# Performance work log

Hardware: AMD Instinct MI355X
Metric: run time of the kernel (lower is better)

## Reference

```python
import jax, jax.numpy as jnp
import numpy as np

CHAN = 256
KEY_DIM = 64
VALUE_DIM = 64
HEADS = 8


def _conv1x1(x, W, b):
    # x: [b,c,h,w], W: [out,c], b: [out]  (1x1 conv == channel matmul)
    return jnp.einsum('bchw,oc->bohw', x, W) + b[None, :, None, None]


def setup_inputs() -> dict:
    key = jax.random.key(0)
    ks = jax.random.split(key, 9)
    qk_out = KEY_DIM * HEADS
    v_out = VALUE_DIM * HEADS
    s_in = 1.0 / np.sqrt(CHAN)
    s_out = 1.0 / np.sqrt(v_out)
    return {
        'x': jax.random.normal(ks[0], (16, CHAN, 64, 64), dtype=jnp.float32),
        'Wq': jax.random.uniform(ks[1], (qk_out, CHAN), jnp.float32, -s_in, s_in),
        'bq': jax.random.uniform(ks[2], (qk_out,), jnp.float32, -s_in, s_in),
        'Wk': jax.random.uniform(ks[3], (qk_out, CHAN), jnp.float32, -s_in, s_in),
        'bk': jax.random.uniform(ks[4], (qk_out,), jnp.float32, -s_in, s_in),
        'Wv': jax.random.uniform(ks[5], (v_out, CHAN), jnp.float32, -s_in, s_in),
        'bv': jax.random.uniform(ks[6], (v_out,), jnp.float32, -s_in, s_in),
        'Wo': jax.random.uniform(ks[7], (CHAN, v_out), jnp.float32, -s_out, s_out),
        'bo': jax.random.uniform(ks[8], (CHAN,), jnp.float32, -s_out, s_out),
    }


def reference(x, Wq, bq, Wk, bk, Wv, bv, Wo, bo):
    b, c, h, w = x.shape
    n = h * w
    scale = KEY_DIM ** (-0.25)
    q = _conv1x1(x, Wq, bq).reshape(b, HEADS, KEY_DIM, n) * scale
    k = _conv1x1(x, Wk, bk).reshape(b, HEADS, KEY_DIM, n) * scale
    v = _conv1x1(x, Wv, bv).reshape(b, HEADS, VALUE_DIM, n)
    k = jax.nn.softmax(k, axis=-1)       # over positions n
    q = jax.nn.softmax(q, axis=-2)       # over key_dim d (norm_queries=True)
    ctx = jnp.einsum('bhdn,bhen->bhde', k, v)   # [b,h,d,e] small context
    out = jnp.einsum('bhdn,bhde->bhen', q, ctx) # [b,h,e,n]
    out = out.reshape(b, HEADS * VALUE_DIM, h, w)
    return _conv1x1(out, Wo, bo)
```

## Files before the change

### kernel.cpp

```cpp
#include <hip/hip_runtime.h>
#include <hip/hip_bf16.h>

typedef unsigned short u16;
typedef unsigned int u32;
typedef __attribute__((ext_vector_type(8))) short bf16x8;
typedef __attribute__((ext_vector_type(4))) float f32x4;

#define NB 16
#define NHEADS 8
#define NPOS 4096
#define QK_SCALE 0.35355339059327373f

__device__ __forceinline__ float bf2f(u32 u) {
  union { u32 i; float f; } x; x.i = u << 16; return x.f;
}
__device__ __forceinline__ u16 f2bf(float f) {
  union { float f; u32 i; } x; x.f = f;
  u32 r = x.i + 0x7fffu + ((x.i >> 16) & 1u);
  return (u16)(r >> 16);
}
__device__ __forceinline__ void unpack8(uint4 r, float* v) {
  v[0] = bf2f(r.x & 0xffffu); v[1] = bf2f(r.x >> 16);
  v[2] = bf2f(r.y & 0xffffu); v[3] = bf2f(r.y >> 16);
  v[4] = bf2f(r.z & 0xffffu); v[5] = bf2f(r.z >> 16);
  v[6] = bf2f(r.w & 0xffffu); v[7] = bf2f(r.w >> 16);
}

__device__ __forceinline__ void async16(u16* ldst, const u16* gsrc) {
  __builtin_amdgcn_global_load_lds(
      (const __attribute__((address_space(1))) unsigned int*)gsrc,
      (__attribute__((address_space(3))) unsigned int*)ldst, 16, 0, 0);
}

__global__ __launch_bounds__(256) void transpose_x(const float* __restrict__ x,
                                                   u16* __restrict__ xT) {
  int b = blockIdx.z;
  int c0 = blockIdx.y * 64;
  int n0 = blockIdx.x * 64;
  const float* xp = x + ((long)b * 256 + c0) * 4096 + n0;
  u16* op = xT + ((long)b * 4096 + n0) * 256 + c0;
  __shared__ float T[64][65];
  int t = threadIdx.x;
  {
    int cl = t >> 2, nc = (t & 3) * 16;
    #pragma unroll
    for (int u = 0; u < 4; ++u) {
      float4 v = *(const float4*)&xp[(long)cl * 4096 + nc + u * 4];
      T[nc + u*4 + 0][cl] = v.x; T[nc + u*4 + 1][cl] = v.y;
      T[nc + u*4 + 2][cl] = v.z; T[nc + u*4 + 3][cl] = v.w;
    }
  }
  __syncthreads();
  {
    int nl = t >> 2, cc = (t & 3) * 16;
    u32 wv[8];
    #pragma unroll
    for (int j = 0; j < 8; ++j)
      wv[j] = (u32)f2bf(T[nl][cc + 2*j]) | ((u32)f2bf(T[nl][cc + 2*j + 1]) << 16);
    *(uint4*)&op[(long)nl * 256 + cc]     = make_uint4(wv[0], wv[1], wv[2], wv[3]);
    *(uint4*)&op[(long)nl * 256 + cc + 8] = make_uint4(wv[4], wv[5], wv[6], wv[7]);
  }
}

__global__ __launch_bounds__(256) void convert_w(
    const float* __restrict__ w0, const float* __restrict__ w1, const float* __restrict__ w2,
    u16* __restrict__ o0, u16* __restrict__ o1, u16* __restrict__ o2) {
  int gid = blockIdx.x * 256 + threadIdx.x;
  int which = gid >> 13;
  int off = (gid & 8191) * 16;
  const float* src = (which == 0) ? w0 : (which == 1) ? w1 : w2;
  u16* dst = (which == 0) ? o0 : (which == 1) ? o1 : o2;
  u32 wv[8];
  #pragma unroll
  for (int u = 0; u < 2; ++u) {
    float4 a = *(const float4*)&src[off + u*8];
    float4 b = *(const float4*)&src[off + u*8 + 4];
    wv[u*4+0] = (u32)f2bf(a.x) | ((u32)f2bf(a.y) << 16);
    wv[u*4+1] = (u32)f2bf(a.z) | ((u32)f2bf(a.w) << 16);
    wv[u*4+2] = (u32)f2bf(b.x) | ((u32)f2bf(b.y) << 16);
    wv[u*4+3] = (u32)f2bf(b.z) | ((u32)f2bf(b.w) << 16);
  }
  *(uint4*)&dst[off]     = make_uint4(wv[0], wv[1], wv[2], wv[3]);
  *(uint4*)&dst[off + 8] = make_uint4(wv[4], wv[5], wv[6], wv[7]);
}

template<int OUT_MODE>
__global__ __launch_bounds__(256) void mfma_gemm(
    const u16* __restrict__ A, long aBatch,
    const u16* __restrict__ B, long bBatch,
    const float* __restrict__ bias,
    void* __restrict__ Cv, long cBatch,
    int K, float scale)
{
  int b = blockIdx.z;
  A += (long)b * aBatch;
  B += (long)b * bBatch;
  int m0 = blockIdx.y * 128, n0 = blockIdx.x * 128;

  __shared__ u16 sm[16384];
  int t = threadIdx.x, w = t >> 6, l = t & 63;
  int lr = l & 15, lk = l >> 4;
  int wr = w >> 1, wcq = w & 1;

  f32x4 acc[4][4];
  #pragma unroll
  for (int i = 0; i < 4; ++i)
    #pragma unroll
    for (int j = 0; j < 4; ++j)
      acc[i][j] = (f32x4){0.f, 0.f, 0.f, 0.f};

  int srow8 = l >> 3;
  int ksl = ((l & 7) ^ (l >> 3)) * 8;

  int nkt = K >> 6;
  for (int kt = 0; kt < nkt; ++kt) {
    int k0 = kt << 6;
    __syncthreads();
    #pragma unroll
    for (int i = 0; i < 4; ++i) {
      int seg = w * 4 + i;
      int row = seg * 8 + srow8;
      async16(&sm[seg * 512], A + (long)(m0 + row) * K + k0 + ksl);
    }
    #pragma unroll
    for (int i = 0; i < 4; ++i) {
      int seg = w * 4 + i;
      int row = seg * 8 + srow8;
      async16(&sm[8192 + seg * 512], B + (long)(n0 + row) * K + k0 + ksl);
    }
    __syncthreads();
    #pragma unroll
    for (int s = 0; s < 2; ++s) {
      bf16x8 af[4], bf[4];
      #pragma unroll
      for (int mi = 0; mi < 4; ++mi) {
        int row = wr * 64 + mi * 16 + lr;
        int slot = (s * 4 + lk) ^ (row & 7);
        af[mi] = *(const bf16x8*)&sm[row * 64 + slot * 8];
      }
      #pragma unroll
      for (int ni = 0; ni < 4; ++ni) {
        int row = wcq * 64 + ni * 16 + lr;
        int slot = (s * 4 + lk) ^ (row & 7);
        bf[ni] = *(const bf16x8*)&sm[8192 + row * 64 + slot * 8];
      }
      #pragma unroll
      for (int mi = 0; mi < 4; ++mi)
        #pragma unroll
        for (int ni = 0; ni < 4; ++ni)
          acc[mi][ni] = __builtin_amdgcn_mfma_f32_16x16x32_bf16(af[mi], bf[ni], acc[mi][ni], 0, 0, 0);
    }
  }

  if (OUT_MODE == 1) {
    u16* Cq = (u16*)Cv + (long)b * cBatch;
    #pragma unroll
    for (int mi = 0; mi < 4; ++mi) {
      int mb = m0 + wr * 64 + mi * 16 + lk * 4;
      float b0 = bias[mb], b1 = bias[mb+1], b2 = bias[mb+2], b3 = bias[mb+3];
      #pragma unroll
      for (int ni = 0; ni < 4; ++ni) {
        int n = n0 + wcq * 64 + ni * 16 + lr;
        f32x4 v = acc[mi][ni];
        ushort4 o;
        o.x = f2bf((v[0] + b0) * scale); o.y = f2bf((v[1] + b1) * scale);
        o.z = f2bf((v[2] + b2) * scale); o.w = f2bf((v[3] + b3) * scale);
        *(ushort4*)&Cq[(long)n * 512 + mb] = o;
      }
    }
  } else if (OUT_MODE == 0) {
    u16* Cb = (u16*)Cv + (long)b * cBatch;
    #pragma unroll
    for (int mi = 0; mi < 4; ++mi)
      #pragma unroll
      for (int r = 0; r < 4; ++r) {
        int m = m0 + wr * 64 + mi * 16 + lk * 4 + r;
        float bi = bias[m];
        #pragma unroll
        for (int ni = 0; ni < 4; ++ni) {
          int n = n0 + wcq * 64 + ni * 16 + lr;
          Cb[(long)m * NPOS + n] = f2bf((acc[mi][ni][r] + bi) * scale);
        }
      }
  } else {
    float* Cf = (float*)Cv + (long)b * cBatch;
    #pragma unroll
    for (int mi = 0; mi < 4; ++mi)
      #pragma unroll
      for (int r = 0; r < 4; ++r) {
        int m = m0 + wr * 64 + mi * 16 + lk * 4 + r;
        float bi = bias[m];
        #pragma unroll
        for (int ni = 0; ni < 4; ++ni) {
          int n = n0 + wcq * 64 + ni * 16 + lr;
          Cf[(long)m * NPOS + n] = acc[mi][ni][r] + bi;
        }
      }
  }
}

__global__ __launch_bounds__(256) void softmax_n(u16* __restrict__ kd) {
  long row = blockIdx.x;
  u16* p = kd + row * NPOS;
  int tid = threadIdx.x;
  int lane = tid & 63, wid = tid >> 6;

  float v[16];
  uint4 r0 = *(const uint4*)(p + tid * 16);
  uint4 r1 = *(const uint4*)(p + tid * 16 + 8);
  unpack8(r0, v); unpack8(r1, v + 8);

  float mx = -1e30f;
  #pragma unroll
  for (int u = 0; u < 16; ++u) mx = fmaxf(mx, v[u]);
  #pragma unroll
  for (int off = 32; off > 0; off >>= 1) mx = fmaxf(mx, __shfl_xor(mx, off));
  __shared__ float smx[4], ssum[4];
  if (lane == 0) smx[wid] = mx;
  __syncthreads();
  mx = fmaxf(fmaxf(smx[0], smx[1]), fmaxf(smx[2], smx[3]));

  float s = 0.f;
  #pragma unroll
  for (int u = 0; u < 16; ++u) { v[u] = __expf(v[u] - mx); s += v[u]; }
  #pragma unroll
  for (int off = 32; off > 0; off >>= 1) s += __shfl_xor(s, off);
  if (lane == 0) ssum[wid] = s;
  __syncthreads();
  s = ssum[0] + ssum[1] + ssum[2] + ssum[3];
  float inv = 1.f / s;

  uint4 o0, o1;
  o0.x = (u32)f2bf(v[0]*inv)  | ((u32)f2bf(v[1]*inv)  << 16);
  o0.y = (u32)f2bf(v[2]*inv)  | ((u32)f2bf(v[3]*inv)  << 16);
  o0.z = (u32)f2bf(v[4]*inv)  | ((u32)f2bf(v[5]*inv)  << 16);
  o0.w = (u32)f2bf(v[6]*inv)  | ((u32)f2bf(v[7]*inv)  << 16);
  o1.x = (u32)f2bf(v[8]*inv)  | ((u32)f2bf(v[9]*inv)  << 16);
  o1.y = (u32)f2bf(v[10]*inv) | ((u32)f2bf(v[11]*inv) << 16);
  o1.z = (u32)f2bf(v[12]*inv) | ((u32)f2bf(v[13]*inv) << 16);
  o1.w = (u32)f2bf(v[14]*inv) | ((u32)f2bf(v[15]*inv) << 16);
  *(uint4*)(p + tid * 16) = o0;
  *(uint4*)(p + tid * 16 + 8) = o1;
}

__global__ __launch_bounds__(64) void ctx_mfma(
    const u16* __restrict__ ksm, const u16* __restrict__ vv, float* __restrict__ ctxp) {
  int ns = blockIdx.x;
  int bh = blockIdx.y;
  const u16* kp = ksm + (long)bh * 64 * NPOS + ns * 256;
  const u16* vp = vv  + (long)bh * 64 * NPOS + ns * 256;
  int l = threadIdx.x;
  int lr = l & 15, lk = l >> 4;
  f32x4 acc[4][4];
  #pragma unroll
  for (int i = 0; i < 4; ++i)
    #pragma unroll
    for (int j = 0; j < 4; ++j)
      acc[i][j] = (f32x4){0.f, 0.f, 0.f, 0.f};

  #pragma unroll 2
  for (int s = 0; s < 8; ++s) {
    int nn = s * 32 + lk * 8;
    bf16x8 a[4], bb[4];
    #pragma unroll
    for (int mi = 0; mi < 4; ++mi)
      a[mi] = *(const bf16x8*)(kp + (long)(mi * 16 + lr) * NPOS + nn);
    #pragma unroll
    for (int ni = 0; ni < 4; ++ni)
      bb[ni] = *(const bf16x8*)(vp + (long)(ni * 16 + lr) * NPOS + nn);
    #pragma unroll
    for (int mi = 0; mi < 4; ++mi)
      #pragma unroll
      for (int ni = 0; ni < 4; ++ni)
        acc[mi][ni] = __builtin_amdgcn_mfma_f32_16x16x32_bf16(a[mi], bb[ni], acc[mi][ni], 0, 0, 0);
  }
  float* cp = ctxp + ((long)ns * 128 + bh) * 4096;
  #pragma unroll
  for (int mi = 0; mi < 4; ++mi)
    #pragma unroll
    for (int ni = 0; ni < 4; ++ni)
      #pragma unroll
      for (int r = 0; r < 4; ++r)
        cp[(mi * 16 + lk * 4 + r) * 64 + ni * 16 + lr] = acc[mi][ni][r];
}

__global__ __launch_bounds__(256) void wc_kernel(
    const float* __restrict__ ctxp, const float* __restrict__ Wo, u16* __restrict__ Wc)
{
  int bh = blockIdx.x;
  int bb = bh >> 3, h = bh & 7;
  __shared__ float Cs[64][65];
  __shared__ float Ws[64][65];
  int tid = threadIdx.x, tx = tid & 15, ty = tid >> 4;

  {
    int row = tid >> 2;
    int ec  = (tid & 3) << 4;
    #pragma unroll
    for (int u = 0; u < 4; ++u) {
      float4 s = make_float4(0, 0, 0, 0);
      #pragma unroll
      for (int si = 0; si < 16; ++si) {
        float4 tv = *(const float4*)&ctxp[(((long)si * 128 + bh) * 64 + row) * 64 + ec + u * 4];
        s.x += tv.x; s.y += tv.y; s.z += tv.z; s.w += tv.w;
      }
      Cs[row][ec + u*4 + 0] = s.x; Cs[row][ec + u*4 + 1] = s.y;
      Cs[row][ec + u*4 + 2] = s.z; Cs[row][ec + u*4 + 3] = s.w;
    }
  }
  for (int cc = 0; cc < 4; ++cc) {
    __syncthreads();
    {
      int row = tid >> 2;
      int ec  = (tid & 3) << 4;
      #pragma unroll
      for (int u = 0; u < 4; ++u) {
        float4 wv = *(const float4*)&Wo[(long)(cc * 64 + row) * 512 + h * 64 + ec + u * 4];
        Ws[row][ec + u*4 + 0] = wv.x; Ws[row][ec + u*4 + 1] = wv.y;
        Ws[row][ec + u*4 + 2] = wv.z; Ws[row][ec + u*4 + 3] = wv.w;
      }
    }
    __syncthreads();
    float acc[4][4] = {};
    #pragma unroll 8
    for (int e = 0; e < 64; ++e) {
      float a[4], b[4];
      #pragma unroll
      for (int i = 0; i < 4; ++i) a[i] = Ws[(ty << 2) + i][e];
      #pragma unroll
      for (int j = 0; j < 4; ++j) b[j] = Cs[(tx << 2) + j][e];
      #pragma unroll
      for (int i = 0; i < 4; ++i)
        #pragma unroll
        for (int j = 0; j < 4; ++j)
          acc[i][j] += a[i] * b[j];
    }
    #pragma unroll
    for (int i = 0; i < 4; ++i) {
      int co = cc * 64 + (ty << 2) + i;
      ushort4 o;
      o.x = f2bf(acc[i][0]); o.y = f2bf(acc[i][1]);
      o.z = f2bf(acc[i][2]); o.w = f2bf(acc[i][3]);
      *(ushort4*)&Wc[((long)bb * 256 + co) * 512 + h * 64 + (tx << 2)] = o;
    }
  }
}

__global__ __launch_bounds__(256) void softmax_d_t(u16* __restrict__ qT) {
  long gid = (long)blockIdx.x * 256 + threadIdx.x;
  u16* p = qT + gid * 64;
  float v[64];
  #pragma unroll
  for (int u = 0; u < 8; ++u) {
    uint4 r = *(const uint4*)(p + u * 8);
    unpack8(r, v + u * 8);
  }
  float mx = -1e30f;
  #pragma unroll
  for (int d = 0; d < 64; ++d) mx = fmaxf(mx, v[d]);
  float s = 0.f;
  #pragma unroll
  for (int d = 0; d < 64; ++d) { v[d] = __expf(v[d] - mx); s += v[d]; }
  float inv = 1.f / s;
  #pragma unroll
  for (int u = 0; u < 8; ++u) {
    uint4 o;
    o.x = (u32)f2bf(v[u*8+0]*inv) | ((u32)f2bf(v[u*8+1]*inv) << 16);
    o.y = (u32)f2bf(v[u*8+2]*inv) | ((u32)f2bf(v[u*8+3]*inv) << 16);
    o.z = (u32)f2bf(v[u*8+4]*inv) | ((u32)f2bf(v[u*8+5]*inv) << 16);
    o.w = (u32)f2bf(v[u*8+6]*inv) | ((u32)f2bf(v[u*8+7]*inv) << 16);
    *(uint4*)(p + u * 8) = o;
  }
}

extern "C" void kernel_launch(void* const* d_in, const int* in_sizes, int n_in,
                              void* d_out, int out_size, void* d_ws, size_t ws_size,
                              hipStream_t stream) {
  (void)in_sizes; (void)n_in; (void)out_size; (void)ws_size;
  const float* x  = (const float*)d_in[0];
  const float* Wq = (const float*)d_in[1];
  const float* bq = (const float*)d_in[2];
  const float* Wk = (const float*)d_in[3];
  const float* bk = (const float*)d_in[4];
  const float* Wv = (const float*)d_in[5];
  const float* bv = (const float*)d_in[6];
  const float* Wo = (const float*)d_in[7];
  const float* bo = (const float*)d_in[8];
  float* out = (float*)d_out;

  char* ws = (char*)d_ws;
  u16*   xT   = (u16*)(ws);
  float* ctxp = (float*)(ws);
  u16*   qT   = (u16*)(ws + 33554432L);
  u16*   kb   = (u16*)(ws + 100663296L);
  u16*   Wcb  = (u16*)(ws + 167772160L);
  u16*   Wqb  = (u16*)(ws + 171966464L);
  u16*   Wkb  = (u16*)(ws + 172228608L);
  u16*   Wvb  = (u16*)(ws + 172490752L);
  u16*   vb   = (u16*)d_out;

  dim3 blk(256);
  long bBx = (long)NPOS * 256;
  long cBqkv = (long)512 * NPOS;
  long cBqT = (long)NPOS * 512;

  hipLaunchKernelGGL(transpose_x, dim3(64, 4, NB), blk, 0, stream, x, xT);
  hipLaunchKernelGGL(convert_w, dim3(96), blk, 0, stream, Wq, Wk, Wv, Wqb, Wkb, Wvb);

  hipLaunchKernelGGL(HIP_KERNEL_NAME(mfma_gemm<1>), dim3(32, 4, NB), blk, 0, stream,
                     Wqb, 0L, xT, bBx, bq, (void*)qT, cBqT, 256, QK_SCALE);
  hipLaunchKernelGGL(HIP_KERNEL_NAME(mfma_gemm<0>), dim3(32, 4, NB), blk, 0, stream,
                     Wkb, 0L, xT, bBx, bk, (void*)kb, cBqkv, 256, QK_SCALE);
  hipLaunchKernelGGL(HIP_KERNEL_NAME(mfma_gemm<0>), dim3(32, 4, NB), blk, 0, stream,
                     Wvb, 0L, xT, bBx, bv, (void*)vb, cBqkv, 256, 1.0f);

  hipLaunchKernelGGL(softmax_n, dim3(NB * 512), blk, 0, stream, kb);
  hipLaunchKernelGGL(ctx_mfma, dim3(16, NB * NHEADS), dim3(64), 0, stream, kb, vb, ctxp);
  hipLaunchKernelGGL(wc_kernel, dim3(NB * NHEADS), blk, 0, stream, ctxp, Wo, Wcb);
  hipLaunchKernelGGL(softmax_d_t, dim3(NB * NPOS * NHEADS / 256), blk, 0, stream, qT);

  hipLaunchKernelGGL(HIP_KERNEL_NAME(mfma_gemm<2>), dim3(32, 2, NB), blk, 0, stream,
                     Wcb, (long)256 * 512, qT, cBqT, bo, (void*)out, (long)256 * NPOS,
                     512, 1.0f);
}
```

Before: 359.4 us.

## Fuse QKV projections with softmaxes and defer key normalization into context

Merges the three QKV projection GEMMs into one launch with a concatenated weight matrix that has the scale folded in. The query softmax over key_dim is computed in the GEMM epilogue via cross-lane shuffles, and the key softmax's exponent is applied there too. The key normalizer is accumulated with an MFMA against a ones vector in the context kernel and divided out in wc_kernel. This removes the separate softmax passes and their round trips through memory. Both GEMMs also gain double-buffered LDS staging. Skipping the max subtraction risks exp overflow for large keys, and bf16 storage of unnormalized exponentials loses some precision.

```diff
diff --git a/kernel.cpp b/kernel.cpp
--- a/kernel.cpp
+++ b/kernel.cpp
@@ -7,7 +7,6 @@
 typedef __attribute__((ext_vector_type(4))) float f32x4;
 
 #define NB 16
-#define NHEADS 8
 #define NPOS 4096
 #define QK_SCALE 0.35355339059327373f
 
@@ -18,12 +17,6 @@
   union { float f; u32 i; } x; x.f = f;
   u32 r = x.i + 0x7fffu + ((x.i >> 16) & 1u);
   return (u16)(r >> 16);
-}
-__device__ __forceinline__ void unpack8(uint4 r, float* v) {
-  v[0] = bf2f(r.x & 0xffffu); v[1] = bf2f(r.x >> 16);
-  v[2] = bf2f(r.y & 0xffffu); v[3] = bf2f(r.y >> 16);
-  v[4] = bf2f(r.z & 0xffffu); v[5] = bf2f(r.z >> 16);
-  v[6] = bf2f(r.w & 0xffffu); v[7] = bf2f(r.w >> 16);
 }
 
 __device__ __forceinline__ void async16(u16* ldst, const u16* gsrc) {
@@ -62,201 +55,198 @@
   }
 }
 
-__global__ __launch_bounds__(256) void convert_w(
-    const float* __restrict__ w0, const float* __restrict__ w1, const float* __restrict__ w2,
-    u16* __restrict__ o0, u16* __restrict__ o1, u16* __restrict__ o2) {
-  int gid = blockIdx.x * 256 + threadIdx.x;
-  int which = gid >> 13;
-  int off = (gid & 8191) * 16;
-  const float* src = (which == 0) ? w0 : (which == 1) ? w1 : w2;
-  u16* dst = (which == 0) ? o0 : (which == 1) ? o1 : o2;
-  u32 wv[8];
-  #pragma unroll
-  for (int u = 0; u < 2; ++u) {
-    float4 a = *(const float4*)&src[off + u*8];
-    float4 b = *(const float4*)&src[off + u*8 + 4];
-    wv[u*4+0] = (u32)f2bf(a.x) | ((u32)f2bf(a.y) << 16);
-    wv[u*4+1] = (u32)f2bf(a.z) | ((u32)f2bf(a.w) << 16);
-    wv[u*4+2] = (u32)f2bf(b.x) | ((u32)f2bf(b.y) << 16);
-    wv[u*4+3] = (u32)f2bf(b.z) | ((u32)f2bf(b.w) << 16);
-  }
-  *(uint4*)&dst[off]     = make_uint4(wv[0], wv[1], wv[2], wv[3]);
-  *(uint4*)&dst[off + 8] = make_uint4(wv[4], wv[5], wv[6], wv[7]);
-}
-
-template<int OUT_MODE>
-__global__ __launch_bounds__(256) void mfma_gemm(
-    const u16* __restrict__ A, long aBatch,
-    const u16* __restrict__ B, long bBatch,
-    const float* __restrict__ bias,
-    void* __restrict__ Cv, long cBatch,
-    int K, float scale)
+__global__ __launch_bounds__(256) void convert_wqkv(
+    const float* __restrict__ Wq, const float* __restrict__ Wk, const float* __restrict__ Wv,
+    const float* __restrict__ bq, const float* __restrict__ bk, const float* __restrict__ bv,
+    u16* __restrict__ W, float* __restrict__ bias)
+{
+  if (blockIdx.x < 96) {
+    int gid = blockIdx.x * 256 + threadIdx.x;
+    int which = gid >> 13;
+    int off = (gid & 8191) * 16;
+    const float* src = which == 0 ? Wq : which == 1 ? Wk : Wv;
+    float scl = which == 2 ? 1.0f : QK_SCALE;
+    u16* dst = W + which * 131072;
+    u32 wv_[8];
+    #pragma unroll
+    for (int u = 0; u < 4; ++u) {
+      float4 a = *(const float4*)&src[off + u * 4];
+      wv_[u*2+0] = (u32)f2bf(a.x*scl) | ((u32)f2bf(a.y*scl) << 16);
+      wv_[u*2+1] = (u32)f2bf(a.z*scl) | ((u32)f2bf(a.w*scl) << 16);
+    }
+    *(uint4*)&dst[off]     = make_uint4(wv_[0], wv_[1], wv_[2], wv_[3]);
+    *(uint4*)&dst[off + 8] = make_uint4(wv_[4], wv_[5], wv_[6], wv_[7]);
+  } else {
+    int t = threadIdx.x;
+    #pragma unroll
+    for (int u = 0; u < 6; ++u) {
+      int i = t * 6 + u;
+      if (i < 1536) {
+        int which = i >> 9, r = i & 511;
+        float v = which == 0 ? bq[r] : which == 1 ? bk[r] : bv[r];
+        bias[i] = which == 2 ? v : v * QK_SCALE;
+      }
+    }
+  }
+}
+
+__global__ __launch_bounds__(256) void proj_qkv(
+    const u16* __restrict__ W, const float* __restrict__ bias,
+    const u16* __restrict__ xT, u16* __restrict__ qT,
+    u16* __restrict__ kx, u16* __restrict__ vb)
 {
   int b = blockIdx.z;
-  A += (long)b * aBatch;
-  B += (long)b * bBatch;
-  int m0 = blockIdx.y * 128, n0 = blockIdx.x * 128;
-
-  __shared__ u16 sm[16384];
+  const u16* Bm = xT + (long)b * (4096L * 256);
+  int mb = blockIdx.y;
+  int m0 = mb * 128, n0 = blockIdx.x * 128;
+
+  __shared__ u16 sm[32768];
   int t = threadIdx.x, w = t >> 6, l = t & 63;
   int lr = l & 15, lk = l >> 4;
   int wr = w >> 1, wcq = w & 1;
+  int srow8 = l >> 3;
+  int ksl = ((l & 7) ^ srow8) * 8;
 
   f32x4 acc[4][4];
   #pragma unroll
   for (int i = 0; i < 4; ++i)
     #pragma unroll
-    for (int j = 0; j < 4; ++j)
-      acc[i][j] = (f32x4){0.f, 0.f, 0.f, 0.f};
-
-  int srow8 = l >> 3;
-  int ksl = ((l & 7) ^ (l >> 3)) * 8;
-
-  int nkt = K >> 6;
-  for (int kt = 0; kt < nkt; ++kt) {
-    int k0 = kt << 6;
-    __syncthreads();
-    #pragma unroll
-    for (int i = 0; i < 4; ++i) {
-      int seg = w * 4 + i;
-      int row = seg * 8 + srow8;
-      async16(&sm[seg * 512], A + (long)(m0 + row) * K + k0 + ksl);
-    }
-    #pragma unroll
-    for (int i = 0; i < 4; ++i) {
-      int seg = w * 4 + i;
-      int row = seg * 8 + srow8;
-      async16(&sm[8192 + seg * 512], B + (long)(n0 + row) * K + k0 + ksl);
-    }
-    __syncthreads();
-    #pragma unroll
-    for (int s = 0; s < 2; ++s) {
-      bf16x8 af[4], bf[4];
-      #pragma unroll
-      for (int mi = 0; mi < 4; ++mi) {
-        int row = wr * 64 + mi * 16 + lr;
-        int slot = (s * 4 + lk) ^ (row & 7);
-        af[mi] = *(const bf16x8*)&sm[row * 64 + slot * 8];
-      }
-      #pragma unroll
-      for (int ni = 0; ni < 4; ++ni) {
-        int row = wcq * 64 + ni * 16 + lr;
-        int slot = (s * 4 + lk) ^ (row & 7);
-        bf[ni] = *(const bf16x8*)&sm[8192 + row * 64 + slot * 8];
-      }
+    for (int j = 0; j < 4; ++j) acc[i][j] = (f32x4){0.f, 0.f, 0.f, 0.f};
+
+#define STAGE_P(buf, kt) { \
+    u16* base_ = sm + (buf) * 16384; \
+    int k0_ = (kt) * 64; \
+    _Pragma("unroll") \
+    for (int i_ = 0; i_ < 4; ++i_) { \
+      int seg_ = w * 4 + i_; \
+      int row_ = seg_ * 8 + srow8; \
+      async16(base_ + seg_ * 512, W + (long)(m0 + row_) * 256 + k0_ + ksl); \
+      async16(base_ + 8192 + seg_ * 512, Bm + (long)(n0 + row_) * 256 + k0_ + ksl); \
+    } }
+
+#define COMPUTE_P(buf) { \
+    const u16* base_ = sm + (buf) * 16384; \
+    _Pragma("unroll") \
+    for (int s_ = 0; s_ < 2; ++s_) { \
+      bf16x8 af_[4], bf_[4]; \
+      _Pragma("unroll") \
+      for (int mi_ = 0; mi_ < 4; ++mi_) { \
+        int row_ = wr * 64 + mi_ * 16 + lr; \
+        int slot_ = (s_ * 4 + lk) ^ (row_ & 7); \
+        af_[mi_] = *(const bf16x8*)&base_[row_ * 64 + slot_ * 8]; \
+      } \
+      _Pragma("unroll") \
+      for (int ni_ = 0; ni_ < 4; ++ni_) { \
+        int row_ = wcq * 64 + ni_ * 16 + lr; \
+        int slot_ = (s_ * 4 + lk) ^ (row_ & 7); \
+        bf_[ni_] = *(const bf16x8*)&base_[8192 + row_ * 64 + slot_ * 8]; \
+      } \
+      _Pragma("unroll") \
+      for (int mi_ = 0; mi_ < 4; ++mi_) \
+        _Pragma("unroll") \
+        for (int ni_ = 0; ni_ < 4; ++ni_) \
+          acc[mi_][ni_] = __builtin_amdgcn_mfma_f32_16x16x32_bf16(af_[mi_], bf_[ni_], acc[mi_][ni_], 0, 0, 0); \
+    } }
+
+#define WAITBAR asm volatile("s_waitcnt vmcnt(0)" ::: "memory"); __builtin_amdgcn_s_barrier();
+
+  STAGE_P(0, 0)
+  WAITBAR
+  STAGE_P(1, 1)
+  COMPUTE_P(0)
+  WAITBAR
+  STAGE_P(0, 2)
+  COMPUTE_P(1)
+  WAITBAR
+  STAGE_P(1, 3)
+  COMPUTE_P(0)
+  WAITBAR
+  COMPUTE_P(1)
+
+  int mbase = m0 + wr * 64;
+  int nbase = n0 + wcq * 64;
+
+  if (mb < 4) {
+    float bv_[4][4];
+    #pragma unroll
+    for (int mi = 0; mi < 4; ++mi)
+      #pragma unroll
+      for (int r = 0; r < 4; ++r) bv_[mi][r] = bias[mbase + mi * 16 + lk * 4 + r];
+    u16* qp = qT + (long)b * (4096L * 512);
+    #pragma unroll
+    for (int ni = 0; ni < 4; ++ni) {
+      float ssum = 0.f;
       #pragma unroll
       for (int mi = 0; mi < 4; ++mi)
         #pragma unroll
-        for (int ni = 0; ni < 4; ++ni)
-          acc[mi][ni] = __builtin_amdgcn_mfma_f32_16x16x32_bf16(af[mi], bf[ni], acc[mi][ni], 0, 0, 0);
-    }
-  }
-
-  if (OUT_MODE == 1) {
-    u16* Cq = (u16*)Cv + (long)b * cBatch;
-    #pragma unroll
-    for (int mi = 0; mi < 4; ++mi) {
-      int mb = m0 + wr * 64 + mi * 16 + lk * 4;
-      float b0 = bias[mb], b1 = bias[mb+1], b2 = bias[mb+2], b3 = bias[mb+3];
-      #pragma unroll
-      for (int ni = 0; ni < 4; ++ni) {
-        int n = n0 + wcq * 64 + ni * 16 + lr;
-        f32x4 v = acc[mi][ni];
+        for (int r = 0; r < 4; ++r) {
+          float e = __expf(acc[mi][ni][r] + bv_[mi][r]);
+          acc[mi][ni][r] = e; ssum += e;
+        }
+      ssum += __shfl_xor(ssum, 16);
+      ssum += __shfl_xor(ssum, 32);
+      float inv = 1.f / ssum;
+      int n = nbase + ni * 16 + lr;
+      #pragma unroll
+      for (int mi = 0; mi < 4; ++mi) {
         ushort4 o;
-        o.x = f2bf((v[0] + b0) * scale); o.y = f2bf((v[1] + b1) * scale);
-        o.z = f2bf((v[2] + b2) * scale); o.w = f2bf((v[3] + b3) * scale);
-        *(ushort4*)&Cq[(long)n * 512 + mb] = o;
-      }
-    }
-  } else if (OUT_MODE == 0) {
-    u16* Cb = (u16*)Cv + (long)b * cBatch;
+        o.x = f2bf(acc[mi][ni][0] * inv); o.y = f2bf(acc[mi][ni][1] * inv);
+        o.z = f2bf(acc[mi][ni][2] * inv); o.w = f2bf(acc[mi][ni][3] * inv);
+        *(ushort4*)&qp[(long)n * 512 + mbase + mi * 16 + lk * 4] = o;
+      }
+    }
+  } else if (mb < 8) {
+    u16* kp = kx + (long)b * (512L * 4096) + (long)(mbase - 512) * 4096;
     #pragma unroll
     for (int mi = 0; mi < 4; ++mi)
       #pragma unroll
       for (int r = 0; r < 4; ++r) {
-        int m = m0 + wr * 64 + mi * 16 + lk * 4 + r;
-        float bi = bias[m];
+        int mr = mi * 16 + lk * 4 + r;
+        float bi = bias[mbase + mr];
         #pragma unroll
         for (int ni = 0; ni < 4; ++ni) {
-          int n = n0 + wcq * 64 + ni * 16 + lr;
-          Cb[(long)m * NPOS + n] = f2bf((acc[mi][ni][r] + bi) * scale);
+          int n = nbase + ni * 16 + lr;
+          kp[(long)mr * 4096 + n] = f2bf(__expf(acc[mi][ni][r] + bi));
         }
       }
   } else {
-    float* Cf = (float*)Cv + (long)b * cBatch;
+    u16* vp = vb + (long)b * (512L * 4096) + (long)(mbase - 1024) * 4096;
     #pragma unroll
     for (int mi = 0; mi < 4; ++mi)
       #pragma unroll
       for (int r = 0; r < 4; ++r) {
-        int m = m0 + wr * 64 + mi * 16 + lk * 4 + r;
-        float bi = bias[m];
+        int mr = mi * 16 + lk * 4 + r;
+        float bi = bias[mbase + mr];
         #pragma unroll
         for (int ni = 0; ni < 4; ++ni) {
-          int n = n0 + wcq * 64 + ni * 16 + lr;
-          Cf[(long)m * NPOS + n] = acc[mi][ni][r] + bi;
+          int n = nbase + ni * 16 + lr;
+          vp[(long)mr * 4096 + n] = f2bf(acc[mi][ni][r] + bi);
         }
       }
   }
-}
-
-__global__ __launch_bounds__(256) void softmax_n(u16* __restrict__ kd) {
-  long row = blockIdx.x;
-  u16* p = kd + row * NPOS;
-  int tid = threadIdx.x;
-  int lane = tid & 63, wid = tid >> 6;
-
-  float v[16];
-  uint4 r0 = *(const uint4*)(p + tid * 16);
-  uint4 r1 = *(const uint4*)(p + tid * 16 + 8);
-  unpack8(r0, v); unpack8(r1, v + 8);
-
-  float mx = -1e30f;
-  #pragma unroll
-  for (int u = 0; u < 16; ++u) mx = fmaxf(mx, v[u]);
-  #pragma unroll
-  for (int off = 32; off > 0; off >>= 1) mx = fmaxf(mx, __shfl_xor(mx, off));
-  __shared__ float smx[4], ssum[4];
-  if (lane == 0) smx[wid] = mx;
-  __syncthreads();
-  mx = fmaxf(fmaxf(smx[0], smx[1]), fmaxf(smx[2], smx[3]));
-
-  float s = 0.f;
-  #pragma unroll
-  for (int u = 0; u < 16; ++u) { v[u] = __expf(v[u] - mx); s += v[u]; }
-  #pragma unroll
-  for (int off = 32; off > 0; off >>= 1) s += __shfl_xor(s, off);
-  if (lane == 0) ssum[wid] = s;
-  __syncthreads();
-  s = ssum[0] + ssum[1] + ssum[2] + ssum[3];
-  float inv = 1.f / s;
-
-  uint4 o0, o1;
-  o0.x = (u32)f2bf(v[0]*inv)  | ((u32)f2bf(v[1]*inv)  << 16);
-  o0.y = (u32)f2bf(v[2]*inv)  | ((u32)f2bf(v[3]*inv)  << 16);
-  o0.z = (u32)f2bf(v[4]*inv)  | ((u32)f2bf(v[5]*inv)  << 16);
-  o0.w = (u32)f2bf(v[6]*inv)  | ((u32)f2bf(v[7]*inv)  << 16);
-  o1.x = (u32)f2bf(v[8]*inv)  | ((u32)f2bf(v[9]*inv)  << 16);
-  o1.y = (u32)f2bf(v[10]*inv) | ((u32)f2bf(v[11]*inv) << 16);
-  o1.z = (u32)f2bf(v[12]*inv) | ((u32)f2bf(v[13]*inv) << 16);
-  o1.w = (u32)f2bf(v[14]*inv) | ((u32)f2bf(v[15]*inv) << 16);
-  *(uint4*)(p + tid * 16) = o0;
-  *(uint4*)(p + tid * 16 + 8) = o1;
+#undef STAGE_P
+#undef COMPUTE_P
 }
 
 __global__ __launch_bounds__(64) void ctx_mfma(
-    const u16* __restrict__ ksm, const u16* __restrict__ vv, float* __restrict__ ctxp) {
+    const u16* __restrict__ kx, const u16* __restrict__ vv,
+    float* __restrict__ Sp, float* __restrict__ Zp)
+{
   int ns = blockIdx.x;
   int bh = blockIdx.y;
-  const u16* kp = ksm + (long)bh * 64 * NPOS + ns * 256;
-  const u16* vp = vv  + (long)bh * 64 * NPOS + ns * 256;
-  int l = threadIdx.x;
-  int lr = l & 15, lk = l >> 4;
-  f32x4 acc[4][4];
-  #pragma unroll
-  for (int i = 0; i < 4; ++i)
-    #pragma unroll
-    for (int j = 0; j < 4; ++j)
-      acc[i][j] = (f32x4){0.f, 0.f, 0.f, 0.f};
+  const u16* kp = kx + (long)bh * 64 * NPOS + ns * 256;
+  const u16* vp = vv + (long)bh * 64 * NPOS + ns * 256;
+  int l = threadIdx.x, lr = l & 15, lk = l >> 4;
+  f32x4 acc[4][4]; f32x4 az[4];
+  #pragma unroll
+  for (int i = 0; i < 4; ++i) {
+    az[i] = (f32x4){0.f, 0.f, 0.f, 0.f};
+    #pragma unroll
+    for (int j = 0; j < 4; ++j) acc[i][j] = (f32x4){0.f, 0.f, 0.f, 0.f};
+  }
+  bf16x8 ones;
+  #pragma unroll
+  for (int j = 0; j < 8; ++j) ones[j] = (short)0x3F80;
 
   #pragma unroll 2
   for (int s = 0; s < 8; ++s) {
@@ -270,22 +260,34 @@
       bb[ni] = *(const bf16x8*)(vp + (long)(ni * 16 + lr) * NPOS + nn);
     #pragma unroll
     for (int mi = 0; mi < 4; ++mi)
+      az[mi] = __builtin_amdgcn_mfma_f32_16x16x32_bf16(a[mi], ones, az[mi], 0, 0, 0);
+    #pragma unroll
+    for (int mi = 0; mi < 4; ++mi)
       #pragma unroll
       for (int ni = 0; ni < 4; ++ni)
         acc[mi][ni] = __builtin_amdgcn_mfma_f32_16x16x32_bf16(a[mi], bb[ni], acc[mi][ni], 0, 0, 0);
   }
-  float* cp = ctxp + ((long)ns * 128 + bh) * 4096;
+  float* sp = Sp + ((long)ns * 128 + bh) * 4096;
   #pragma unroll
   for (int mi = 0; mi < 4; ++mi)
     #pragma unroll
     for (int ni = 0; ni < 4; ++ni)
       #pragma unroll
       for (int r = 0; r < 4; ++r)
-        cp[(mi * 16 + lk * 4 + r) * 64 + ni * 16 + lr] = acc[mi][ni][r];
+        sp[(mi * 16 + lk * 4 + r) * 64 + ni * 16 + lr] = acc[mi][ni][r];
+  if (lr == 0) {
+    float* zp = Zp + ((long)ns * 128 + bh) * 64;
+    #pragma unroll
+    for (int mi = 0; mi < 4; ++mi)
+      #pragma unroll
+      for (int r = 0; r < 4; ++r)
+        zp[mi * 16 + lk * 4 + r] = az[mi][r];
+  }
 }
 
 __global__ __launch_bounds__(256) void wc_kernel(
-    const float* __restrict__ ctxp, const float* __restrict__ Wo, u16* __restrict__ Wc)
+    const float* __restrict__ Sp, const float* __restrict__ Zp,
+    const float* __restrict__ Wo, u16* __restrict__ Wc)
 {
   int bh = blockIdx.x;
   int bb = bh >> 3, h = bh & 7;
@@ -296,16 +298,20 @@
   {
     int row = tid >> 2;
     int ec  = (tid & 3) << 4;
+    float Zr = 0.f;
+    #pragma unroll
+    for (int si = 0; si < 16; ++si) Zr += Zp[((long)si * 128 + bh) * 64 + row];
+    float invZ = 1.f / Zr;
     #pragma unroll
     for (int u = 0; u < 4; ++u) {
       float4 s = make_float4(0, 0, 0, 0);
       #pragma unroll
       for (int si = 0; si < 16; ++si) {
-        float4 tv = *(const float4*)&ctxp[(((long)si * 128 + bh) * 64 + row) * 64 + ec + u * 4];
+        float4 tv = *(const float4*)&Sp[(((long)si * 128 + bh) * 64 + row) * 64 + ec + u * 4];
         s.x += tv.x; s.y += tv.y; s.z += tv.z; s.w += tv.w;
       }
-      Cs[row][ec + u*4 + 0] = s.x; Cs[row][ec + u*4 + 1] = s.y;
-      Cs[row][ec + u*4 + 2] = s.z; Cs[row][ec + u*4 + 3] = s.w;
+      Cs[row][ec + u*4 + 0] = s.x * invZ; Cs[row][ec + u*4 + 1] = s.y * invZ;
+      Cs[row][ec + u*4 + 2] = s.z * invZ; Cs[row][ec + u*4 + 3] = s.w * invZ;
     }
   }
   for (int cc = 0; cc < 4; ++cc) {
@@ -346,31 +352,91 @@
   }
 }
 
-__global__ __launch_bounds__(256) void softmax_d_t(u16* __restrict__ qT) {
-  long gid = (long)blockIdx.x * 256 + threadIdx.x;
-  u16* p = qT + gid * 64;
-  float v[64];
-  #pragma unroll
-  for (int u = 0; u < 8; ++u) {
-    uint4 r = *(const uint4*)(p + u * 8);
-    unpack8(r, v + u * 8);
-  }
-  float mx = -1e30f;
-  #pragma unroll
-  for (int d = 0; d < 64; ++d) mx = fmaxf(mx, v[d]);
-  float s = 0.f;
-  #pragma unroll
-  for (int d = 0; d < 64; ++d) { v[d] = __expf(v[d] - mx); s += v[d]; }
-  float inv = 1.f / s;
-  #pragma unroll
-  for (int u = 0; u < 8; ++u) {
-    uint4 o;
-    o.x = (u32)f2bf(v[u*8+0]*inv) | ((u32)f2bf(v[u*8+1]*inv) << 16);
-    o.y = (u32)f2bf(v[u*8+2]*inv) | ((u32)f2bf(v[u*8+3]*inv) << 16);
-    o.z = (u32)f2bf(v[u*8+4]*inv) | ((u32)f2bf(v[u*8+5]*inv) << 16);
-    o.w = (u32)f2bf(v[u*8+6]*inv) | ((u32)f2bf(v[u*8+7]*inv) << 16);
-    *(uint4*)(p + u * 8) = o;
-  }
+__global__ __launch_bounds__(256) void final_gemm(
+    const u16* __restrict__ Wc, const u16* __restrict__ qTg,
+    const float* __restrict__ bo, float* __restrict__ out)
+{
+  int b = blockIdx.z;
+  const u16* A = Wc + (long)b * (256L * 512);
+  const u16* Bm = qTg + (long)b * (4096L * 512);
+  int m0 = blockIdx.y * 128, n0 = blockIdx.x * 128;
+
+  __shared__ u16 sm[32768];
+  int t = threadIdx.x, w = t >> 6, l = t & 63;
+  int lr = l & 15, lk = l >> 4;
+  int wr = w >> 1, wcq = w & 1;
+  int srow8 = l >> 3;
+  int ksl = ((l & 7) ^ srow8) * 8;
+
+  f32x4 acc[4][4];
+  #pragma unroll
+  for (int i = 0; i < 4; ++i)
+    #pragma unroll
+    for (int j = 0; j < 4; ++j) acc[i][j] = (f32x4){0.f, 0.f, 0.f, 0.f};
+
+#define STAGE_F(buf, kt) { \
+    u16* base_ = sm + (buf) * 16384; \
+    int k0_ = (kt) * 64; \
+    _Pragma("unroll") \
+    for (int i_ = 0; i_ < 4; ++i_) { \
+      int seg_ = w * 4 + i_; \
+      int row_ = seg_ * 8 + srow8; \
+      async16(base_ + seg_ * 512, A + (long)(m0 + row_) * 512 + k0_ + ksl); \
+      async16(base_ + 8192 + seg_ * 512, Bm + (long)(n0 + row_) * 512 + k0_ + ksl); \
+    } }
+
+#define COMPUTE_F(buf) { \
+    const u16* base_ = sm + (buf) * 16384; \
+    _Pragma("unroll") \
+    for (int s_ = 0; s_ < 2; ++s_) { \
+      bf16x8 af_[4], bf_[4]; \
+      _Pragma("unroll") \
+      for (int mi_ = 0; mi_ < 4; ++mi_) { \
+        int row_ = wr * 64 + mi_ * 16 + lr; \
+        int slot_ = (s_ * 4 + lk) ^ (row_ & 7); \
+        af_[mi_] = *(const bf16x8*)&base_[row_ * 64 + slot_ * 8]; \
+      } \
+      _Pragma("unroll") \
+      for (int ni_ = 0; ni_ < 4; ++ni_) { \
+        int row_ = wcq * 64 + ni_ * 16 + lr; \
+        int slot_ = (s_ * 4 + lk) ^ (row_ & 7); \
+        bf_[ni_] = *(const bf16x8*)&base_[8192 + row_ * 64 + slot_ * 8]; \
+      } \
+      _Pragma("unroll") \
+      for (int mi_ = 0; mi_ < 4; ++mi_) \
+        _Pragma("unroll") \
+        for (int ni_ = 0; ni_ < 4; ++ni_) \
+          acc[mi_][ni_] = __builtin_amdgcn_mfma_f32_16x16x32_bf16(af_[mi_], bf_[ni_], acc[mi_][ni_], 0, 0, 0); \
+    } }
+
+  STAGE_F(0, 0)
+  WAITBAR
+  #pragma unroll
+  for (int kt = 0; kt < 8; ++kt) {
+    if (kt < 7) {
+      if ((kt & 1) == 0) { STAGE_F(1, kt + 1) } else { STAGE_F(0, kt + 1) }
+    }
+    if ((kt & 1) == 0) { COMPUTE_F(0) } else { COMPUTE_F(1) }
+    if (kt < 7) { WAITBAR }
+  }
+
+  float* op = out + (long)b * (256L * 4096);
+  int mbase = m0 + wr * 64;
+  int nbase = n0 + wcq * 64;
+  #pragma unroll
+  for (int mi = 0; mi < 4; ++mi)
+    #pragma unroll
+    for (int r = 0; r < 4; ++r) {
+      int m = mbase + mi * 16 + lk * 4 + r;
+      float bi = bo[m];
+      #pragma unroll
+      for (int ni = 0; ni < 4; ++ni) {
+        int n = nbase + ni * 16 + lr;
+        op[(long)m * 4096 + n] = acc[mi][ni][r] + bi;
+      }
+    }
+#undef STAGE_F
+#undef COMPUTE_F
 }
 
 extern "C" void kernel_launch(void* const* d_in, const int* in_sizes, int n_in,
@@ -389,37 +455,21 @@
   float* out = (float*)d_out;
 
   char* ws = (char*)d_ws;
-  u16*   xT   = (u16*)(ws);
-  float* ctxp = (float*)(ws);
-  u16*   qT   = (u16*)(ws + 33554432L);
-  u16*   kb   = (u16*)(ws + 100663296L);
-  u16*   Wcb  = (u16*)(ws + 167772160L);
-  u16*   Wqb  = (u16*)(ws + 171966464L);
-  u16*   Wkb  = (u16*)(ws + 172228608L);
-  u16*   Wvb  = (u16*)(ws + 172490752L);
-  u16*   vb   = (u16*)d_out;
+  u16*   xT    = (u16*)(ws);
+  float* Sp    = (float*)(ws);
+  u16*   qT    = (u16*)(ws + 33554432L);
+  u16*   kx    = (u16*)(ws + 100663296L);
+  u16*   Wcb   = (u16*)(ws + 167772160L);
+  u16*   Wqkvb = (u16*)(ws + 171966464L);
+  float* bqkv  = (float*)(ws + 172752896L);
+  float* Zp    = (float*)(ws + 172759040L);
+  u16*   vb    = (u16*)d_out;
 
   dim3 blk(256);
-  long bBx = (long)NPOS * 256;
-  long cBqkv = (long)512 * NPOS;
-  long cBqT = (long)NPOS * 512;
-
   hipLaunchKernelGGL(transpose_x, dim3(64, 4, NB), blk, 0, stream, x, xT);
-  hipLaunchKernelGGL(convert_w, dim3(96), blk, 0, stream, Wq, Wk, Wv, Wqb, Wkb, Wvb);
-
-  hipLaunchKernelGGL(HIP_KERNEL_NAME(mfma_gemm<1>), dim3(32, 4, NB), blk, 0, stream,
-                     Wqb, 0L, xT, bBx, bq, (void*)qT, cBqT, 256, QK_SCALE);
-  hipLaunchKernelGGL(HIP_KERNEL_NAME(mfma_gemm<0>), dim3(32, 4, NB), blk, 0, stream,
-                     Wkb, 0L, xT, bBx, bk, (void*)kb, cBqkv, 256, QK_SCALE);
-  hipLaunchKernelGGL(HIP_KERNEL_NAME(mfma_gemm<0>), dim3(32, 4, NB), blk, 0, stream,
-                     Wvb, 0L, xT, bBx, bv, (void*)vb, cBqkv, 256, 1.0f);
-
-  hipLaunchKernelGGL(softmax_n, dim3(NB * 512), blk, 0, stream, kb);
-  hipLaunchKernelGGL(ctx_mfma, dim3(16, NB * NHEADS), dim3(64), 0, stream, kb, vb, ctxp);
-  hipLaunchKernelGGL(wc_kernel, dim3(NB * NHEADS), blk, 0, stream, ctxp, Wo, Wcb);
-  hipLaunchKernelGGL(softmax_d_t, dim3(NB * NPOS * NHEADS / 256), blk, 0, stream, qT);
-
-  hipLaunchKernelGGL(HIP_KERNEL_NAME(mfma_gemm<2>), dim3(32, 2, NB), blk, 0, stream,
-                     Wcb, (long)256 * 512, qT, cBqT, bo, (void*)out, (long)256 * NPOS,
-                     512, 1.0f);
-}
+  hipLaunchKernelGGL(convert_wqkv, dim3(97), blk, 0, stream, Wq, Wk, Wv, bq, bk, bv, Wqkvb, bqkv);
+  hipLaunchKernelGGL(proj_qkv, dim3(32, 12, NB), blk, 0, stream, Wqkvb, bqkv, xT, qT, kx, vb);
+  hipLaunchKernelGGL(ctx_mfma, dim3(16, 128), dim3(64), 0, stream, kx, vb, Sp, Zp);
+  hipLaunchKernelGGL(wc_kernel, dim3(128), blk, 0, stream, Sp, Zp, Wo, Wcb);
+  hipLaunchKernelGGL(final_gemm, dim3(32, 2, NB), blk, 0, stream, Wcb, qT, bo, out);
+}
```

Result: faster. 306.2 us (-14.8%).
